# Kernel tuning notes

Hardware: AMD Instinct MI355X
Metric: run time of the kernel (lower is better)

The kernel has to match this reference:

```python
import jax, jax.numpy as jnp
import numpy as np

B = 131072
N_Q = 4          # qubits -> 16-dim state
N_KER = 4
K, STRIDE, HOUT = 4, 2, 3
EPS = 1e-12


def _rot_mats(w):
    # w: (4,3) -> (4,2,2) complex Rot(phi,theta,omega) = RZ(omega) RY(theta) RZ(phi)
    phi, theta, omega = w[:, 0], w[:, 1], w[:, 2]
    c, s = jnp.cos(theta / 2), jnp.sin(theta / 2)
    ep = jnp.exp(-0.5j * (phi + omega).astype(jnp.complex64))
    em = jnp.exp(0.5j * (phi - omega).astype(jnp.complex64))
    m00 = ep * c
    m01 = -em * s
    m10 = jnp.conj(em) * s
    m11 = jnp.conj(ep) * c
    return jnp.stack([jnp.stack([m00, m01], -1), jnp.stack([m10, m11], -1)], -2)


def _apply_1q(s, U, wire):
    # s: (N,2,2,2,2) with axis 1+wire for each qubit (wire 0 = most significant)
    s = jnp.moveaxis(s, 1 + wire, 1)
    s = jnp.einsum('ij,nj...->ni...', U, s)
    return jnp.moveaxis(s, 1, 1 + wire)


def _apply_cnot(s, c, t):
    c_ax, t_ax = 1 + c, 1 + t
    s0 = jnp.take(s, 0, axis=c_ax)
    s1 = jnp.take(s, 1, axis=c_ax)
    t2 = t_ax - 1 if t_ax > c_ax else t_ax
    s1 = jnp.flip(s1, axis=t2)
    return jnp.stack([s0, s1], axis=c_ax)


def _qkernel(amps, w):
    # amps: (N,16) real L2-normalized; w: (4,3). Returns (N,3) expvals (X,Y,Z) on wire 0.
    s = amps.astype(jnp.complex64).reshape(-1, 2, 2, 2, 2)
    mats = _rot_mats(w)
    for q in range(N_Q):
        s = _apply_1q(s, mats[q], q)
    for q in range(N_Q - 1):
        s = _apply_cnot(s, q, q + 1)
    s = _apply_cnot(s, N_Q - 1, 0)
    s2 = s.reshape(-1, 2, 8)
    a, b = s2[:, 0], s2[:, 1]
    ab = jnp.sum(jnp.conj(a) * b, axis=-1)
    X = 2.0 * jnp.real(ab)
    Y = 2.0 * jnp.imag(ab)
    Z = jnp.sum(jnp.abs(a) ** 2 - jnp.abs(b) ** 2, axis=-1)
    out = jnp.stack([X, Y, Z], axis=-1)
    return jnp.nan_to_num(out, nan=0.0, posinf=1.0, neginf=-1.0)


def _leaky(x):
    return jnp.where(x >= 0, x, 0.1 * x)


def setup_inputs() -> dict:
    key = jax.random.key(0)
    ks = jax.random.split(key, 6)
    return {
        'x': jax.random.normal(ks[0], (B, 1, 8, 8), dtype=jnp.float32),
        'qweights': 0.01 * jax.random.normal(ks[1], (N_KER, N_Q, 3), dtype=jnp.float32),
        'fc1_w': 0.05 * jax.random.normal(ks[2], (32, 108), dtype=jnp.float32),
        'fc1_b': jnp.zeros((32,), dtype=jnp.float32),
        'fc2_w': 0.05 * jax.random.normal(ks[3], (3, 32), dtype=jnp.float32),
        'fc2_b': jnp.zeros((3,), dtype=jnp.float32),
    }


def reference(x, qweights, fc1_w, fc1_b, fc2_w, fc2_b):
    Bsz = x.shape[0]
    x2 = x[:, 0]                                        # (B,8,8)
    idx = (jnp.arange(HOUT) * STRIDE)[:, None] + jnp.arange(K)[None, :]  # (3,4)
    p = x2[:, idx]                                      # (B,3,4,8)
    p = p[:, :, :, idx]                                 # (B,3,4,3,4) = (B,hout,kh,wout,kw)
    p = jnp.transpose(p, (0, 1, 3, 2, 4)).reshape(Bsz * HOUT * HOUT, K * K)
    norms = jnp.linalg.norm(p, axis=-1, keepdims=True) + EPS
    amps = jnp.nan_to_num(p / norms, nan=0.0, posinf=0.0, neginf=0.0)
    feats = jnp.concatenate(
        [_qkernel(amps, qweights[k]).reshape(Bsz, HOUT, HOUT, 3) for k in range(N_KER)],
        axis=-1)                                        # (B,3,3,12)
    feats = jnp.transpose(feats, (0, 3, 1, 2))          # (B,12,3,3)
    feats = jnp.nan_to_num(feats, nan=0.0, posinf=0.0, neginf=0.0)
    h = _leaky(feats).reshape(Bsz, -1)                  # (B,108)
    h = _leaky(h @ fc1_w.T + fc1_b)
    return h @ fc2_w.T + fc2_b                          # (B,3) logits
```

## Files before the change

kernel.cpp:

```cpp
#include <hip/hip_runtime.h>
#include <math.h>


#define QC_EPS 1e-12f

__device__ __forceinline__ float leakyf(float v) { return v >= 0.0f ? v : 0.1f * v; }

__global__ __launch_bounds__(256) void qccnn_fused(
    const float* __restrict__ x,
    const float* __restrict__ qw,
    const float* __restrict__ w1,
    const float* __restrict__ b1,
    const float* __restrict__ w2,
    const float* __restrict__ b2,
    float* __restrict__ out,
    int Bsz)
{
    __shared__ float s_w1t[108][36];
    __shared__ float s_qm[4][4][9];

    const int tid = threadIdx.x;

    for (int idx = tid; idx < 32 * 108; idx += 256) {
        const int o = idx / 108, f = idx % 108;
        s_w1t[f][o] = w1[idx];
    }
    if (tid < 16) {
        const int k = tid >> 2, q = tid & 3;
        const float phi = qw[(k * 4 + q) * 3 + 0];
        const float th  = qw[(k * 4 + q) * 3 + 1];
        const float om  = qw[(k * 4 + q) * 3 + 2];
        float c, s, ca, sa, cb, sb;
        sincosf(0.5f * th, &s, &c);
        sincosf(0.5f * (phi + om), &sa, &ca);
        sincosf(0.5f * (phi - om), &sb, &cb);
        float* M = &s_qm[k][q][0];
        M[0] =  ca * c;  M[1] = -sa * c;
        M[2] = -cb * s;  M[3] = -sb * s;
        M[4] =  cb * s;  M[5] = -sb * s;
        M[6] =  ca * c;  M[7] =  sa * c;
    }
    __syncthreads();

    const int img_l = tid >> 2;
    const int k     = tid & 3;
    const int b     = blockIdx.x * 64 + img_l;
    const bool valid = (b < Bsz);
    const float* xb = x + (size_t)b * 64;

    float h[32];
#pragma unroll
    for (int o = 0; o < 32; ++o) h[o] = 0.0f;

    constexpr int PERM[16] = {0, 13, 3, 14, 6, 11, 5, 8, 12, 1, 15, 2, 10, 7, 9, 4};

    int pi = 0, pj = 0;
#pragma unroll 1
    for (int pt = 0; pt < 9; ++pt) {
        float p[16];
        if (valid) {
            const float* pr = xb + pi * 16 + pj * 2;
#pragma unroll
            for (int r = 0; r < 4; ++r) {
                const float2 lo = *reinterpret_cast<const float2*>(pr + r * 8);
                const float2 hi = *reinterpret_cast<const float2*>(pr + r * 8 + 2);
                p[r * 4 + 0] = lo.x; p[r * 4 + 1] = lo.y;
                p[r * 4 + 2] = hi.x; p[r * 4 + 3] = hi.y;
            }
        } else {
#pragma unroll
            for (int l = 0; l < 16; ++l) p[l] = 0.0f;
        }
        float ss = 0.0f;
#pragma unroll
        for (int l = 0; l < 16; ++l) ss += p[l] * p[l];
        const float inv = 1.0f / (sqrtf(ss) + QC_EPS);
#pragma unroll
        for (int l = 0; l < 16; ++l) p[l] *= inv;

        float sr[16], si[16];
        {
            const float* M = &s_qm[k][3][0];
            const float m00r = M[0], m00i = M[1], m01r = M[2], m01i = M[3];
            const float m10r = M[4], m10i = M[5], m11r = M[6], m11i = M[7];
#pragma unroll
            for (int t = 0; t < 8; ++t) {
                const float a0 = p[2 * t], a1 = p[2 * t + 1];
                sr[2 * t]     = m00r * a0 + m01r * a1;
                si[2 * t]     = m00i * a0 + m01i * a1;
                sr[2 * t + 1] = m10r * a0 + m11r * a1;
                si[2 * t + 1] = m10i * a0 + m11i * a1;
            }
        }
#pragma unroll
        for (int g = 0; g < 3; ++g) {
            const int qq = (g == 0) ? 2 : ((g == 1) ? 1 : 0);
            const int m  = (g == 0) ? 2 : ((g == 1) ? 4 : 8);
            const float* M = &s_qm[k][qq][0];
            const float m00r = M[0], m00i = M[1], m01r = M[2], m01i = M[3];
            const float m10r = M[4], m10i = M[5], m11r = M[6], m11i = M[7];
#pragma unroll
            for (int i0 = 0; i0 < 16; ++i0) {
                if (i0 & m) continue;
                const int i1 = i0 | m;
                const float t0r = sr[i0], t0i = si[i0];
                const float t1r = sr[i1], t1i = si[i1];
                sr[i0] = m00r * t0r - m00i * t0i + m01r * t1r - m01i * t1i;
                si[i0] = m00r * t0i + m00i * t0r + m01r * t1i + m01i * t1r;
                sr[i1] = m10r * t0r - m10i * t0i + m11r * t1r - m11i * t1i;
                si[i1] = m10r * t0i + m10i * t0r + m11r * t1i + m11i * t1r;
            }
        }

        float abr = 0.0f, abi = 0.0f, zz = 0.0f;
#pragma unroll
        for (int jj = 0; jj < 8; ++jj) {
            const int ia = PERM[jj], ib = PERM[8 + jj];
            const float ar = sr[ia], ai = si[ia];
            const float br = sr[ib], bi = si[ib];
            abr += ar * br + ai * bi;
            abi += ar * bi - ai * br;
            zz  += (ar * ar + ai * ai) - (br * br + bi * bi);
        }

        {
            const float f0 = leakyf(2.0f * abr);
            const float f1 = leakyf(2.0f * abi);
            const float f2 = leakyf(zz);
            const int fb = k * 27 + pt;
#pragma unroll
            for (int comp = 0; comp < 3; ++comp) {
                const float lf = (comp == 0) ? f0 : ((comp == 1) ? f1 : f2);
                const float* wrow = &s_w1t[fb + comp * 9][0];
#pragma unroll
                for (int o4 = 0; o4 < 8; ++o4) {
                    const float4 wv = *reinterpret_cast<const float4*>(&wrow[o4 * 4]);
                    h[o4 * 4 + 0] += wv.x * lf;
                    h[o4 * 4 + 1] += wv.y * lf;
                    h[o4 * 4 + 2] += wv.z * lf;
                    h[o4 * 4 + 3] += wv.w * lf;
                }
            }
        }

        if (++pj == 3) { pj = 0; ++pi; }
    }

#pragma unroll
    for (int o = 0; o < 32; ++o) {
        h[o] += __shfl_xor(h[o], 1);
        h[o] += __shfl_xor(h[o], 2);
    }

    if (k == 0 && valid) {
        float o0 = b2[0], o1 = b2[1], o2 = b2[2];
#pragma unroll
        for (int o = 0; o < 32; ++o) {
            const float hv = leakyf(h[o] + b1[o]);
            o0 += w2[o] * hv;
            o1 += w2[32 + o] * hv;
            o2 += w2[64 + o] * hv;
        }
        float* ob = out + (size_t)b * 3;
        ob[0] = o0; ob[1] = o1; ob[2] = o2;
    }
}

extern "C" void kernel_launch(void* const* d_in, const int* in_sizes, int n_in,
                              void* d_out, int out_size, void* d_ws, size_t ws_size,
                              hipStream_t stream) {
    (void)n_in; (void)out_size; (void)d_ws; (void)ws_size;
    const float* x  = (const float*)d_in[0];
    const float* qw = (const float*)d_in[1];
    const float* w1 = (const float*)d_in[2];
    const float* b1 = (const float*)d_in[3];
    const float* w2 = (const float*)d_in[4];
    const float* b2 = (const float*)d_in[5];
    float* out = (float*)d_out;

    const int Bsz = in_sizes[0] / 64;
    const int blocks = (Bsz + 63) / 64;

    qccnn_fused<<<blocks, 256, 0, stream>>>(x, qw, w1, b1, w2, b2, out, Bsz);
}
```

Baseline: 155.3 us.

## Defer patch normalization to expvals and split fc1 across lanes via shared features

The patch amplitude normalization is moved out of the state vector and applied once to the quadratic expectation values as 1/norm^2. The first rotation is applied as the input is loaded, and all gate matrices are cached in registers. The fc1 accumulation is restructured: each lane writes its features to a shared-memory feature tile, and after a barrier each of the 4 lanes per image computes 8 of the 32 hidden outputs. The fc2 partial sums are then reduced with shuffles, replacing 32 accumulator registers and 64 shuffles per thread. This adds about 28KB of LDS and a block barrier, which may lower occupancy.

```diff
diff --git a/kernel.cpp b/kernel.cpp
--- a/kernel.cpp
+++ b/kernel.cpp
@@ -16,14 +16,15 @@
     float* __restrict__ out,
     int Bsz)
 {
-    __shared__ float s_w1t[108][36];
+    __shared__ float s_w1[32][116];
+    __shared__ float s_feats[64][112];
     __shared__ float s_qm[4][4][9];
 
     const int tid = threadIdx.x;
 
     for (int idx = tid; idx < 32 * 108; idx += 256) {
         const int o = idx / 108, f = idx % 108;
-        s_w1t[f][o] = w1[idx];
+        s_w1[o][f] = w1[idx];
     }
     if (tid < 16) {
         const int k = tid >> 2, q = tid & 3;
@@ -48,57 +49,48 @@
     const bool valid = (b < Bsz);
     const float* xb = x + (size_t)b * 64;
 
-    float h[32];
+    float M[4][8];
 #pragma unroll
-    for (int o = 0; o < 32; ++o) h[o] = 0.0f;
+    for (int q = 0; q < 4; ++q)
+#pragma unroll
+        for (int e = 0; e < 8; ++e) M[q][e] = s_qm[k][q][e];
 
     constexpr int PERM[16] = {0, 13, 3, 14, 6, 11, 5, 8, 12, 1, 15, 2, 10, 7, 9, 4};
 
     int pi = 0, pj = 0;
 #pragma unroll 1
     for (int pt = 0; pt < 9; ++pt) {
-        float p[16];
+        float sr[16], si[16];
+        float ss = 0.0f;
         if (valid) {
             const float* pr = xb + pi * 16 + pj * 2;
+            const float m00r = M[3][0], m00i = M[3][1], m01r = M[3][2], m01i = M[3][3];
+            const float m10r = M[3][4], m10i = M[3][5], m11r = M[3][6], m11i = M[3][7];
 #pragma unroll
             for (int r = 0; r < 4; ++r) {
                 const float2 lo = *reinterpret_cast<const float2*>(pr + r * 8);
                 const float2 hi = *reinterpret_cast<const float2*>(pr + r * 8 + 2);
-                p[r * 4 + 0] = lo.x; p[r * 4 + 1] = lo.y;
-                p[r * 4 + 2] = hi.x; p[r * 4 + 3] = hi.y;
+                ss += lo.x * lo.x + lo.y * lo.y + hi.x * hi.x + hi.y * hi.y;
+                sr[4 * r + 0] = m00r * lo.x + m01r * lo.y;
+                si[4 * r + 0] = m00i * lo.x + m01i * lo.y;
+                sr[4 * r + 1] = m10r * lo.x + m11r * lo.y;
+                si[4 * r + 1] = m10i * lo.x + m11i * lo.y;
+                sr[4 * r + 2] = m00r * hi.x + m01r * hi.y;
+                si[4 * r + 2] = m00i * hi.x + m01i * hi.y;
+                sr[4 * r + 3] = m10r * hi.x + m11r * hi.y;
+                si[4 * r + 3] = m10i * hi.x + m11i * hi.y;
             }
         } else {
 #pragma unroll
-            for (int l = 0; l < 16; ++l) p[l] = 0.0f;
+            for (int l = 0; l < 16; ++l) { sr[l] = 0.0f; si[l] = 0.0f; }
         }
-        float ss = 0.0f;
-#pragma unroll
-        for (int l = 0; l < 16; ++l) ss += p[l] * p[l];
-        const float inv = 1.0f / (sqrtf(ss) + QC_EPS);
-#pragma unroll
-        for (int l = 0; l < 16; ++l) p[l] *= inv;
 
-        float sr[16], si[16];
-        {
-            const float* M = &s_qm[k][3][0];
-            const float m00r = M[0], m00i = M[1], m01r = M[2], m01i = M[3];
-            const float m10r = M[4], m10i = M[5], m11r = M[6], m11i = M[7];
-#pragma unroll
-            for (int t = 0; t < 8; ++t) {
-                const float a0 = p[2 * t], a1 = p[2 * t + 1];
-                sr[2 * t]     = m00r * a0 + m01r * a1;
-                si[2 * t]     = m00i * a0 + m01i * a1;
-                sr[2 * t + 1] = m10r * a0 + m11r * a1;
-                si[2 * t + 1] = m10i * a0 + m11i * a1;
-            }
-        }
 #pragma unroll
         for (int g = 0; g < 3; ++g) {
             const int qq = (g == 0) ? 2 : ((g == 1) ? 1 : 0);
             const int m  = (g == 0) ? 2 : ((g == 1) ? 4 : 8);
-            const float* M = &s_qm[k][qq][0];
-            const float m00r = M[0], m00i = M[1], m01r = M[2], m01i = M[3];
-            const float m10r = M[4], m10i = M[5], m11r = M[6], m11i = M[7];
+            const float m00r = M[qq][0], m00i = M[qq][1], m01r = M[qq][2], m01i = M[qq][3];
+            const float m10r = M[qq][4], m10i = M[qq][5], m11r = M[qq][6], m11i = M[qq][7];
 #pragma unroll
             for (int i0 = 0; i0 < 16; ++i0) {
                 if (i0 & m) continue;
@@ -124,45 +116,53 @@
         }
 
         {
-            const float f0 = leakyf(2.0f * abr);
-            const float f1 = leakyf(2.0f * abi);
-            const float f2 = leakyf(zz);
-            const int fb = k * 27 + pt;
-#pragma unroll
-            for (int comp = 0; comp < 3; ++comp) {
-                const float lf = (comp == 0) ? f0 : ((comp == 1) ? f1 : f2);
-                const float* wrow = &s_w1t[fb + comp * 9][0];
-#pragma unroll
-                for (int o4 = 0; o4 < 8; ++o4) {
-                    const float4 wv = *reinterpret_cast<const float4*>(&wrow[o4 * 4]);
-                    h[o4 * 4 + 0] += wv.x * lf;
-                    h[o4 * 4 + 1] += wv.y * lf;
-                    h[o4 * 4 + 2] += wv.z * lf;
-                    h[o4 * 4 + 3] += wv.w * lf;
-                }
-            }
+            const float denom = sqrtf(ss) + QC_EPS;
+            const float inv2  = 1.0f / (denom * denom);
+            const float f0 = leakyf(2.0f * abr * inv2);
+            const float f1 = leakyf(2.0f * abi * inv2);
+            const float f2 = leakyf(zz * inv2);
+            float* row = &s_feats[img_l][k * 27 + pt];
+            row[0]  = f0;
+            row[9]  = f1;
+            row[18] = f2;
         }
 
         if (++pj == 3) { pj = 0; ++pi; }
     }
+    __syncthreads();
 
+    float h[8];
 #pragma unroll
-    for (int o = 0; o < 32; ++o) {
-        h[o] += __shfl_xor(h[o], 1);
-        h[o] += __shfl_xor(h[o], 2);
+    for (int j = 0; j < 8; ++j) h[j] = 0.0f;
+
+#pragma unroll 1
+    for (int f4 = 0; f4 < 27; ++f4) {
+        const float4 fv = *reinterpret_cast<const float4*>(&s_feats[img_l][f4 * 4]);
+#pragma unroll
+        for (int j = 0; j < 8; ++j) {
+            const float4 wv = *reinterpret_cast<const float4*>(&s_w1[4 * j + k][f4 * 4]);
+            h[j] += wv.x * fv.x + wv.y * fv.y + wv.z * fv.z + wv.w * fv.w;
+        }
     }
 
+    float o0 = 0.0f, o1 = 0.0f, o2 = 0.0f;
+#pragma unroll
+    for (int j = 0; j < 8; ++j) {
+        const int o = 4 * j + k;
+        const float hv = leakyf(h[j] + b1[o]);
+        o0 += w2[o] * hv;
+        o1 += w2[32 + o] * hv;
+        o2 += w2[64 + o] * hv;
+    }
+    o0 += __shfl_xor(o0, 1);  o0 += __shfl_xor(o0, 2);
+    o1 += __shfl_xor(o1, 1);  o1 += __shfl_xor(o1, 2);
+    o2 += __shfl_xor(o2, 1);  o2 += __shfl_xor(o2, 2);
+
     if (k == 0 && valid) {
-        float o0 = b2[0], o1 = b2[1], o2 = b2[2];
-#pragma unroll
-        for (int o = 0; o < 32; ++o) {
-            const float hv = leakyf(h[o] + b1[o]);
-            o0 += w2[o] * hv;
-            o1 += w2[32 + o] * hv;
-            o2 += w2[64 + o] * hv;
-        }
         float* ob = out + (size_t)b * 3;
-        ob[0] = o0; ob[1] = o1; ob[2] = o2;
+        ob[0] = o0 + b2[0];
+        ob[1] = o1 + b2[1];
+        ob[2] = o2 + b2[2];
     }
 }
 
```

Result: slower. 169.4 us (+9.1%).
